# Performance work log

Measured on AMD Instinct MI355X. Metric: run time of the kernel, lower is better.

## Reference

```python
import jax, jax.numpy as jnp
import numpy as np

B, S, H, V = 16, 128, 512, 50000
N, R = 5, 2          # mem_size, read_heads
Wd = H               # memory cell width
EPS = 1e-6
XI_SIZES = [R * Wd, R, Wd, 1, Wd, Wd, R, 1, 1, 3 * R]
XI = int(np.sum(XI_SIZES))  # 2573


def oneplus(x):
    return 1.0 + jax.nn.softplus(x)


def content_weight(M, k, beta):
    # M: [B,N,Wd], k: [B,R,Wd], beta: [B,R] -> [B,R,N]
    Mn = M / (jnp.linalg.norm(M, axis=-1, keepdims=True) + EPS)
    kn = k / (jnp.linalg.norm(k, axis=-1, keepdims=True) + EPS)
    sim = jnp.einsum('brw,bnw->brn', kn, Mn)
    return jax.nn.softmax(beta[:, :, None] * sim, axis=-1)


def setup_inputs() -> dict:
    key = jax.random.key(0)
    ks = jax.random.split(key, 8)
    emb = jax.random.normal(ks[0], (V, H), jnp.float32) * 0.02
    emb = emb.at[0].set(0.0)  # PAD row
    return {
        'source': jax.random.randint(ks[1], (B, S), 0, V),
        'source_lengths': jax.random.randint(ks[2], (B,), 1, S + 1),
        'emb': emb,
        'W_ih': jax.random.normal(ks[3], (4 * H, H + R * Wd), jnp.float32) * 0.02,
        'W_hh': jax.random.normal(ks[4], (4 * H, H), jnp.float32) * 0.02,
        'b_lstm': jnp.zeros((4 * H,), jnp.float32),
        'W_int': jax.random.normal(ks[5], (H, XI), jnp.float32) * 0.02,
        'b_int': jnp.zeros((XI,), jnp.float32),
        'W_out': jax.random.normal(ks[6], (H + R * Wd, H), jnp.float32) * 0.02,
        'b_out': jnp.zeros((H,), jnp.float32),
    }


def dnc_forward(source, emb, W_ih, W_hh, b_lstm, W_int, b_int, W_out, b_out):
    x_emb = emb[source]  # [B,S,H] embedding lookup
    splits = np.cumsum(XI_SIZES)[:-1]
    eye = jnp.eye(N, dtype=jnp.float32)

    def step(carry, x_t):
        h, c, M, u, p, L, wr, ww, r = carry
        # LSTM controller: input = [embedded token; read vectors]
        xin = jnp.concatenate([x_t, r.reshape(-1, R * Wd)], axis=-1)
        gates = xin @ W_ih.T + h @ W_hh.T + b_lstm
        i_, f_, g_, o_ = jnp.split(gates, 4, axis=-1)
        c = jax.nn.sigmoid(f_) * c + jax.nn.sigmoid(i_) * jnp.tanh(g_)
        h = jax.nn.sigmoid(o_) * jnp.tanh(c)
        # interface vector
        xi = h @ W_int + b_int
        (rk, rb, wk, wb, e, v, fg, ga, gw, pi) = jnp.split(xi, splits, axis=-1)
        rk = rk.reshape(-1, R, Wd)
        rb = oneplus(rb)                       # [B,R]
        wb = oneplus(wb)                       # [B,1]
        e = jax.nn.sigmoid(e)                  # [B,Wd]
        fg = jax.nn.sigmoid(fg)                # [B,R]
        ga = jax.nn.sigmoid(ga)                # [B,1]
        gw = jax.nn.sigmoid(gw)                # [B,1]
        pi = jax.nn.softmax(pi.reshape(-1, R, 3), axis=-1)
        # usage / retention
        psi = jnp.prod(1.0 - fg[:, :, None] * wr, axis=1)        # [B,N]
        u = (u + ww - u * ww) * psi
        # allocation weighting (sort-based, irregular access)
        phi = jnp.argsort(u, axis=-1)
        u_s = jnp.take_along_axis(u, phi, axis=-1)
        excl = jnp.concatenate([jnp.ones_like(u_s[:, :1]), jnp.cumprod(u_s, axis=-1)[:, :-1]], axis=-1)
        a_s = (1.0 - u_s) * excl
        a = jnp.take_along_axis(a_s, jnp.argsort(phi, axis=-1), axis=-1)
        # write weighting
        cw = content_weight(M, wk[:, None, :], wb)[:, 0]         # [B,N]
        ww = gw * (ga * a + (1.0 - ga) * cw)
        # memory write
        M = M * (1.0 - ww[:, :, None] * e[:, None, :]) + ww[:, :, None] * v[:, None, :]
        # temporal link matrix + precedence
        L = (1.0 - ww[:, :, None] - ww[:, None, :]) * L + ww[:, :, None] * p[:, None, :]
        L = L * (1.0 - eye)
        p = (1.0 - ww.sum(-1, keepdims=True)) * p + ww
        # read weightings
        fw = jnp.einsum('bij,brj->bri', L, wr)
        bw = jnp.einsum('bji,brj->bri', L, wr)
        cr = content_weight(M, rk, rb)                           # [B,R,N]
        wr = pi[..., 0:1] * bw + pi[..., 1:2] * cr + pi[..., 2:3] * fw
        r = jnp.einsum('brn,bnw->brw', wr, M)                    # [B,R,Wd]
        out_t = jnp.concatenate([h, r.reshape(-1, R * Wd)], axis=-1) @ W_out + b_out
        return (h, c, M, u, p, L, wr, ww, r), out_t

    z = jnp.zeros
    init = (z((B, H)), z((B, H)), z((B, N, Wd)), z((B, N)), z((B, N)),
            z((B, N, N)), z((B, R, N)), z((B, N)), z((B, R, Wd)))
    (h, c, *_), outs = jax.lax.scan(step, init, jnp.swapaxes(x_emb, 0, 1))
    return jnp.swapaxes(outs, 0, 1), h, c


def reference(source, source_lengths, emb, W_ih, W_hh, b_lstm, W_int, b_int, W_out, b_out):
    outputs, h, c = dnc_forward(source, emb, W_ih, W_hh, b_lstm, W_int, b_int, W_out, b_out)
    return outputs, (h, c)
```

## Files before the change

kernel.cpp:

```cpp
#include <hip/hip_runtime.h>
#include <math.h>

#define EPSC 1e-6f
#define NBLK 128

#define OFF_H     0u
#define OFF_R     16384u
#define OFF_FLAGS 32768u
#define OFF_GO    36864u
#define STATE_END 40960u
#define OFF_XI    40960u
#define OFF_GX    90112u
#define OFF_HR    4284416u

typedef float f32x4 __attribute__((ext_vector_type(4)));

__device__ __forceinline__ float sigmf(float x) { return 1.0f / (1.0f + expf(-x)); }
__device__ __forceinline__ float oneplusf(float x) {
    return 1.0f + fmaxf(x, 0.0f) + log1pf(expf(-fabsf(x)));
}

__device__ __forceinline__ void gst(float* p, float v) {
    __hip_atomic_store((unsigned*)p, __float_as_uint(v),
                       __ATOMIC_RELAXED, __HIP_MEMORY_SCOPE_AGENT);
}

__device__ __forceinline__ void cld12(
    f32x4& d0, f32x4& d1, f32x4& d2, f32x4& d3, f32x4& d4, f32x4& d5,
    f32x4& d6, f32x4& d7, f32x4& d8, f32x4& d9, f32x4& d10, f32x4& d11,
    const float* p0, const float* p1, const float* p2, const float* p3,
    const float* p4, const float* p5, const float* p6, const float* p7,
    const float* p8, const float* p9, const float* p10, const float* p11)
{
    asm volatile(
        "global_load_dwordx4 %0, %12, off sc0 sc1\n\t"
        "global_load_dwordx4 %1, %13, off sc0 sc1\n\t"
        "global_load_dwordx4 %2, %14, off sc0 sc1\n\t"
        "global_load_dwordx4 %3, %15, off sc0 sc1\n\t"
        "global_load_dwordx4 %4, %16, off sc0 sc1\n\t"
        "global_load_dwordx4 %5, %17, off sc0 sc1\n\t"
        "global_load_dwordx4 %6, %18, off sc0 sc1\n\t"
        "global_load_dwordx4 %7, %19, off sc0 sc1\n\t"
        "global_load_dwordx4 %8, %20, off sc0 sc1\n\t"
        "global_load_dwordx4 %9, %21, off sc0 sc1\n\t"
        "global_load_dwordx4 %10, %22, off sc0 sc1\n\t"
        "global_load_dwordx4 %11, %23, off sc0 sc1\n\t"
        "s_waitcnt vmcnt(0)"
        : "=&v"(d0), "=&v"(d1), "=&v"(d2), "=&v"(d3), "=&v"(d4), "=&v"(d5),
          "=&v"(d6), "=&v"(d7), "=&v"(d8), "=&v"(d9), "=&v"(d10), "=&v"(d11)
        : "v"(p0), "v"(p1), "v"(p2), "v"(p3), "v"(p4), "v"(p5),
          "v"(p6), "v"(p7), "v"(p8), "v"(p9), "v"(p10), "v"(p11)
        : "memory");
}

__device__ __forceinline__ void cld8(
    f32x4& d0, f32x4& d1, f32x4& d2, f32x4& d3,
    f32x4& d4, f32x4& d5, f32x4& d6, f32x4& d7,
    const float* p0, const float* p1, const float* p2, const float* p3,
    const float* p4, const float* p5, const float* p6, const float* p7)
{
    asm volatile(
        "global_load_dwordx4 %0, %8, off sc0 sc1\n\t"
        "global_load_dwordx4 %1, %9, off sc0 sc1\n\t"
        "global_load_dwordx4 %2, %10, off sc0 sc1\n\t"
        "global_load_dwordx4 %3, %11, off sc0 sc1\n\t"
        "global_load_dwordx4 %4, %12, off sc0 sc1\n\t"
        "global_load_dwordx4 %5, %13, off sc0 sc1\n\t"
        "global_load_dwordx4 %6, %14, off sc0 sc1\n\t"
        "global_load_dwordx4 %7, %15, off sc0 sc1\n\t"
        "s_waitcnt vmcnt(0)"
        : "=&v"(d0), "=&v"(d1), "=&v"(d2), "=&v"(d3),
          "=&v"(d4), "=&v"(d5), "=&v"(d6), "=&v"(d7)
        : "v"(p0), "v"(p1), "v"(p2), "v"(p3),
          "v"(p4), "v"(p5), "v"(p6), "v"(p7)
        : "memory");
}

__device__ __forceinline__ void cld3(
    f32x4& d0, f32x4& d1, f32x4& d2,
    const float* p0, const float* p1, const float* p2)
{
    asm volatile(
        "global_load_dwordx4 %0, %3, off sc0 sc1\n\t"
        "global_load_dwordx4 %1, %4, off sc0 sc1\n\t"
        "global_load_dwordx4 %2, %5, off sc0 sc1\n\t"
        "s_waitcnt vmcnt(0)"
        : "=&v"(d0), "=&v"(d1), "=&v"(d2)
        : "v"(p0), "v"(p1), "v"(p2)
        : "memory");
}

__device__ __forceinline__ void gsync(unsigned* flags, unsigned* go, unsigned gen,
                                      int bi, int tid)
{
    __builtin_amdgcn_s_waitcnt(0);
    __syncthreads();
    if (tid == 0)
        __hip_atomic_store(&flags[bi * 32], gen, __ATOMIC_RELAXED, __HIP_MEMORY_SCOPE_AGENT);
    if (bi == 0) {
        if (tid < NBLK) {
            unsigned v;
            do {
                v = __hip_atomic_load(&flags[tid * 32], __ATOMIC_RELAXED, __HIP_MEMORY_SCOPE_AGENT);
                if (v < gen) __builtin_amdgcn_s_sleep(1);
            } while (v < gen);
        }
        __syncthreads();
        if (tid < NBLK)
            __hip_atomic_store(&go[tid * 32], gen, __ATOMIC_RELAXED, __HIP_MEMORY_SCOPE_AGENT);
    }
    if (tid == 0) {
        unsigned v;
        do {
            v = __hip_atomic_load(&go[bi * 32], __ATOMIC_RELAXED, __HIP_MEMORY_SCOPE_AGENT);
            if (v < gen) __builtin_amdgcn_s_sleep(1);
        } while (v < gen);
    }
    __syncthreads();
}

template <int K>
__device__ __forceinline__ void blk_reduce(float* v, float (*s_red)[20],
                                           float* outp, int tid)
{
#pragma unroll
    for (int i = 0; i < K; i++) {
        float x = v[i];
        for (int o = 32; o > 0; o >>= 1) x += __shfl_down(x, o, 64);
        if ((tid & 63) == 0) s_red[tid >> 6][i] = x;
    }
    __syncthreads();
    if (tid < K) outp[tid] = s_red[0][tid] + s_red[1][tid] + s_red[2][tid] + s_red[3][tid];
    __syncthreads();
}

__global__ __launch_bounds__(256, 1) void k_main(
    const float* __restrict__ W_ih, const float* __restrict__ W_hh,
    const float* __restrict__ W_int, const float* __restrict__ b_int,
    const float* __restrict__ gx, float* __restrict__ hbuf,
    float* __restrict__ rbuf, float* __restrict__ xib,
    float* __restrict__ hr, float* __restrict__ out,
    unsigned* __restrict__ flags, unsigned* __restrict__ go)
{
    const int tid = threadIdx.x;
    const int bi  = blockIdx.x;

    __shared__ __align__(16) float big_u[12288];
    __shared__ float s_part[1024];
    __shared__ float c_s[64];
    __shared__ __align__(16) float s_M[5][520];
    __shared__ float st_u[5], st_p[5], st_L[25], st_wr[10], st_ww[5];
    __shared__ float s_red[4][20];
    __shared__ float s_rb[2], s_wb, s_fg[2], s_ga, s_gw, s_pi[2][3];
    __shared__ float s_wrold[2][5], s_uu[5], s_a[5], s_wwn[5];
    __shared__ float s_pold[5], s_Lnew[25];
    __shared__ float s_zw[5], s_z[2][5], s_fw[2][5], s_bw[2][5];
    __shared__ float s_dotA[11], s_dotB[17], s_wrnew[2][5];

    const int cG  = tid & 15;
    const int ksl = tid >> 4;
    const int cg  = (cG >> 2) * 512 + bi * 4 + (cG & 3);

    if (tid < 64) c_s[tid] = 0.f;
    if (bi < 16) {
        for (int i = tid; i < 5 * 520; i += 256) (&s_M[0][0])[i] = 0.f;
        if (tid < 5)  { st_u[tid] = 0.f; st_p[tid] = 0.f; st_ww[tid] = 0.f; }
        if (tid < 25) st_L[tid] = 0.f;
        if (tid < 10) st_wr[tid] = 0.f;
    }
    __syncthreads();

    unsigned gen = 0;

#pragma unroll 1
    for (int t = 0; t < 128; t++) {
        const float* h_in  = hbuf + (t & 1) * 8192;
        float*       h_out = hbuf + ((t + 1) & 1) * 8192;

        float acc[16];
#pragma unroll
        for (int b = 0; b < 16; b++) acc[b] = 0.f;

#pragma unroll 1
        for (int hf = 0; hf < 2; hf++) {
            {
                const int b  = tid >> 4;
                const int sg = tid & 15;
                const float* pp[12];
#pragma unroll
                for (int i = 0; i < 12; i++) {
                    int kg = hf * 768 + sg * 4 + i * 64;
                    pp[i] = (kg < 512) ? h_in + b * 512 + kg
                                       : rbuf + b * 1024 + (kg - 512);
                }
                f32x4 d0, d1, d2, d3, d4, d5, d6, d7, d8, d9, d10, d11;
                cld12(d0, d1, d2, d3, d4, d5, d6, d7, d8, d9, d10, d11,
                      pp[0], pp[1], pp[2], pp[3], pp[4], pp[5],
                      pp[6], pp[7], pp[8], pp[9], pp[10], pp[11]);
                float* dst = &big_u[b * 768 + sg * 4];
                *(f32x4*)(dst + 0 * 64) = d0;  *(f32x4*)(dst + 1 * 64) = d1;
                *(f32x4*)(dst + 2 * 64) = d2;  *(f32x4*)(dst + 3 * 64) = d3;
                *(f32x4*)(dst + 4 * 64) = d4;  *(f32x4*)(dst + 5 * 64) = d5;
                *(f32x4*)(dst + 6 * 64) = d6;  *(f32x4*)(dst + 7 * 64) = d7;
                *(f32x4*)(dst + 8 * 64) = d8;  *(f32x4*)(dst + 9 * 64) = d9;
                *(f32x4*)(dst + 10 * 64) = d10; *(f32x4*)(dst + 11 * 64) = d11;
            }
            __syncthreads();
#pragma unroll
            for (int i = 0; i < 12; i++) {
                int lc = ksl * 4 + i * 64;
                int kg = hf * 768 + lc;
                const float* wp = (kg < 512) ? W_hh + (size_t)cg * 512 + kg
                                             : W_ih + (size_t)cg * 1536 + kg;
                f32x4 wv = *(const f32x4*)wp;
#pragma unroll
                for (int b = 0; b < 16; b++) {
                    f32x4 xv = *(const f32x4*)&big_u[b * 768 + lc];
                    acc[b] = fmaf(wv[0], xv[0], acc[b]);
                    acc[b] = fmaf(wv[1], xv[1], acc[b]);
                    acc[b] = fmaf(wv[2], xv[2], acc[b]);
                    acc[b] = fmaf(wv[3], xv[3], acc[b]);
                }
            }
            __syncthreads();
        }

#pragma unroll
        for (int b = 0; b < 16; b++) {
            float x = acc[b];
            x += __shfl_xor(x, 16, 64);
            x += __shfl_xor(x, 32, 64);
            acc[b] = x;
        }
        {
            int wv = tid >> 6;
            if ((tid & 63) < 16) {
#pragma unroll
                for (int b = 0; b < 16; b++)
                    s_part[(wv * 16 + cG) * 16 + b] = acc[b];
            }
        }
        __syncthreads();
        {
            int c = tid & 15, b = tid >> 4;
            float tot = s_part[(0 * 16 + c) * 16 + b] + s_part[(1 * 16 + c) * 16 + b]
                      + s_part[(2 * 16 + c) * 16 + b] + s_part[(3 * 16 + c) * 16 + b];
            int cgc = (c >> 2) * 512 + bi * 4 + (c & 3);
            tot += gx[((size_t)t * 16 + b) * 2048 + cgc];
            s_part[c * 16 + b] = tot;
        }
        __syncthreads();
        if (tid < 64) {
            int jl = tid & 3, b = tid >> 2;
            float gi  = s_part[(0 * 4 + jl) * 16 + b];
            float gf  = s_part[(1 * 4 + jl) * 16 + b];
            float gg  = s_part[(2 * 4 + jl) * 16 + b];
            float go_ = s_part[(3 * 4 + jl) * 16 + b];
            float cc = sigmf(gf) * c_s[jl * 16 + b] + sigmf(gi) * tanhf(gg);
            float hh = sigmf(go_) * tanhf(cc);
            c_s[jl * 16 + b] = cc;
            int j = bi * 4 + jl;
            gst(h_out + b * 512 + j, hh);
            hr[((size_t)t * 16 + b) * 1536 + j] = hh;
            if (t == 127) {
                out[1048576 + b * 512 + j] = hh;
                out[1048576 + 8192 + b * 512 + j] = cc;
            }
        }
        gen++;
        gsync(flags, go, gen, bi, tid);

        {
            {
                const int b = tid >> 4, s = tid & 15;
                const float* hp = h_out + b * 512 + s * 4;
                f32x4 d0, d1, d2, d3, d4, d5, d6, d7;
                cld8(d0, d1, d2, d3, d4, d5, d6, d7,
                     hp + 0 * 64, hp + 1 * 64, hp + 2 * 64, hp + 3 * 64,
                     hp + 4 * 64, hp + 5 * 64, hp + 6 * 64, hp + 7 * 64);
                float* dst = &big_u[b * 512 + s * 4];
                *(f32x4*)(dst + 0 * 64) = d0; *(f32x4*)(dst + 1 * 64) = d1;
                *(f32x4*)(dst + 2 * 64) = d2; *(f32x4*)(dst + 3 * 64) = d3;
                *(f32x4*)(dst + 4 * 64) = d4; *(f32x4*)(dst + 5 * 64) = d5;
                *(f32x4*)(dst + 6 * 64) = d6; *(f32x4*)(dst + 7 * 64) = d7;
            }
            __syncthreads();
            const int ql  = tid & 15;
            const int kcl = tid >> 4;
#pragma unroll 1
            for (int p = 0; p < 2; p++) {
                int q0 = p * 2048 + bi * 16;
                if (p == 1 && q0 >= 2573) break;
                int q  = q0 + ql;
                int qc = (q < 2573) ? q : 2572;
                float wxr[32];
#pragma unroll
                for (int i = 0; i < 32; i++)
                    wxr[i] = W_int[(size_t)(kcl * 32 + i) * 2573 + qc];
                float ax[16];
#pragma unroll
                for (int b = 0; b < 16; b++) ax[b] = 0.f;
#pragma unroll
                for (int b = 0; b < 16; b++) {
                    const f32x4* hp = (const f32x4*)&big_u[b * 512 + kcl * 32];
#pragma unroll
                    for (int i4 = 0; i4 < 8; i4++) {
                        f32x4 hv = hp[i4];
                        ax[b] = fmaf(wxr[i4 * 4 + 0], hv[0], ax[b]);
                        ax[b] = fmaf(wxr[i4 * 4 + 1], hv[1], ax[b]);
                        ax[b] = fmaf(wxr[i4 * 4 + 2], hv[2], ax[b]);
                        ax[b] = fmaf(wxr[i4 * 4 + 3], hv[3], ax[b]);
                    }
                }
#pragma unroll
                for (int b = 0; b < 16; b++) {
                    float x = ax[b];
                    x += __shfl_xor(x, 16, 64);
                    x += __shfl_xor(x, 32, 64);
                    ax[b] = x;
                }
                {
                    int wv = tid >> 6;
                    if ((tid & 63) < 16) {
#pragma unroll
                        for (int b = 0; b < 16; b++)
                            s_part[(wv * 16 + ql) * 16 + b] = ax[b];
                    }
                }
                __syncthreads();
                {
                    int q_l = tid >> 4, b = tid & 15;
                    int qq = q0 + q_l;
                    if (qq < 2573) {
                        float v = s_part[(0 + q_l) * 16 + b] + s_part[(16 + q_l) * 16 + b]
                                + s_part[(32 + q_l) * 16 + b] + s_part[(48 + q_l) * 16 + b]
                                + b_int[qq];
                        gst(&xib[b * 3072 + qq], v);
                    }
                }
                __syncthreads();
            }
        }
        gen++;
        gsync(flags, go, gen, bi, tid);

        if (bi < 16) {
            {
                const float* xs = xib + bi * 3072;
                f32x4 d0, d1, d2;
                cld3(d0, d1, d2,
                     xs + (tid + 0) * 4, xs + (tid + 256) * 4, xs + (tid + 512) * 4);
                *(f32x4*)&big_u[(tid + 0) * 4]   = d0;
                *(f32x4*)&big_u[(tid + 256) * 4] = d1;
                *(f32x4*)&big_u[(tid + 512) * 4] = d2;
            }
            __syncthreads();
            const float* xb = big_u;

            if (tid == 0) {
                s_wb = oneplusf(xb[1538]);
                s_ga = sigmf(xb[2565]);
                s_gw = sigmf(xb[2566]);
            }
            if (tid == 1 || tid == 2) {
                int rr = tid - 1;
                s_rb[rr] = oneplusf(xb[1024 + rr]);
                s_fg[rr] = sigmf(xb[2563 + rr]);
                float z0 = xb[2567 + rr * 3], z1 = xb[2568 + rr * 3], z2 = xb[2569 + rr * 3];
                float mx = fmaxf(z0, fmaxf(z1, z2));
                float e0 = expf(z0 - mx), e1 = expf(z1 - mx), e2 = expf(z2 - mx);
                float s = e0 + e1 + e2;
                s_pi[rr][0] = e0 / s; s_pi[rr][1] = e1 / s; s_pi[rr][2] = e2 / s;
            }
            if (tid >= 32 && tid < 42) { int i = tid - 32; s_wrold[i / 5][i % 5] = st_wr[i]; }
            if (tid >= 64 && tid < 69) { s_pold[tid - 64] = st_p[tid - 64]; }
            __syncthreads();
            if (tid < 5) {
                float psi = (1.f - s_fg[0] * s_wrold[0][tid]) * (1.f - s_fg[1] * s_wrold[1][tid]);
                float un = (st_u[tid] + st_ww[tid] - st_u[tid] * st_ww[tid]) * psi;
                s_uu[tid] = un; st_u[tid] = un;
            }
            __syncthreads();
            if (tid < 5) {
                float excl = 1.f;
#pragma unroll
                for (int m2 = 0; m2 < 5; m2++) {
                    bool before = (s_uu[m2] < s_uu[tid]) || (s_uu[m2] == s_uu[tid] && m2 < tid);
                    if (before) excl *= s_uu[m2];
                }
                s_a[tid] = (1.f - s_uu[tid]) * excl;
            }
            float accA[11];
#pragma unroll
            for (int i = 0; i < 11; i++) accA[i] = 0.f;
            for (int w = tid; w < 512; w += 256) {
                float wk = xb[1026 + w];
                accA[10] += wk * wk;
#pragma unroll
                for (int n = 0; n < 5; n++) {
                    float m_ = s_M[n][w];
                    accA[n]     += m_ * m_;
                    accA[5 + n] += wk * m_;
                }
            }
            blk_reduce<11>(accA, s_red, s_dotA, tid);
            if (tid < 5) {
                float sim = s_dotA[5 + tid] /
                            ((sqrtf(s_dotA[10]) + EPSC) * (sqrtf(s_dotA[tid]) + EPSC));
                s_zw[tid] = s_wb * sim;
            }
            __syncthreads();
            if (tid < 5) {
                float mx = s_zw[0];
#pragma unroll
                for (int m2 = 1; m2 < 5; m2++) mx = fmaxf(mx, s_zw[m2]);
                float sum = 0.f;
#pragma unroll
                for (int m2 = 0; m2 < 5; m2++) sum += expf(s_zw[m2] - mx);
                float cw = expf(s_zw[tid] - mx) / sum;
                float w_ = s_gw * (s_ga * s_a[tid] + (1.f - s_ga) * cw);
                s_wwn[tid] = w_; st_ww[tid] = w_;
            }
            __syncthreads();
            float accB[17];
#pragma unroll
            for (int i = 0; i < 17; i++) accB[i] = 0.f;
            for (int w = tid; w < 512; w += 256) {
                float ew = sigmf(xb[1539 + w]);
                float vw = xb[2051 + w];
                float rk0 = xb[w], rk1 = xb[512 + w];
                accB[15] += rk0 * rk0; accB[16] += rk1 * rk1;
#pragma unroll
                for (int n = 0; n < 5; n++) {
                    float m_ = s_M[n][w];
                    float mn_ = m_ * (1.f - s_wwn[n] * ew) + s_wwn[n] * vw;
                    s_M[n][w] = mn_;
                    accB[n]      += mn_ * mn_;
                    accB[5 + n]  += rk0 * mn_;
                    accB[10 + n] += rk1 * mn_;
                }
            }
            blk_reduce<17>(accB, s_red, s_dotB, tid);
            if (tid < 25) {
                int i2 = tid / 5, j2 = tid % 5;
                float Ln = (i2 == j2) ? 0.f
                         : (1.f - s_wwn[i2] - s_wwn[j2]) * st_L[tid] + s_wwn[i2] * s_pold[j2];
                s_Lnew[tid] = Ln; st_L[tid] = Ln;
            }
            __syncthreads();
            if (tid < 5) {
                float wsum = s_wwn[0] + s_wwn[1] + s_wwn[2] + s_wwn[3] + s_wwn[4];
                st_p[tid] = (1.f - wsum) * s_pold[tid] + s_wwn[tid];
            }
            if (tid < 10) {
                int rr = tid / 5, ii = tid % 5;
                float fw = 0.f, bw = 0.f;
#pragma unroll
                for (int j2 = 0; j2 < 5; j2++) {
                    fw += s_Lnew[ii * 5 + j2] * s_wrold[rr][j2];
                    bw += s_Lnew[j2 * 5 + ii] * s_wrold[rr][j2];
                }
                s_fw[rr][ii] = fw; s_bw[rr][ii] = bw;
                float sim = s_dotB[5 + rr * 5 + ii] /
                            ((sqrtf(s_dotB[15 + rr]) + EPSC) * (sqrtf(s_dotB[ii]) + EPSC));
                s_z[rr][ii] = s_rb[rr] * sim;
            }
            __syncthreads();
            if (tid < 10) {
                int rr = tid / 5, ii = tid % 5;
                float mx = s_z[rr][0];
#pragma unroll
                for (int m2 = 1; m2 < 5; m2++) mx = fmaxf(mx, s_z[rr][m2]);
                float sum = 0.f;
#pragma unroll
                for (int m2 = 0; m2 < 5; m2++) sum += expf(s_z[rr][m2] - mx);
                float cr = expf(s_z[rr][ii] - mx) / sum;
                float wn = s_pi[rr][0] * s_bw[rr][ii] + s_pi[rr][1] * cr + s_pi[rr][2] * s_fw[rr][ii];
                s_wrnew[rr][ii] = wn; st_wr[rr * 5 + ii] = wn;
            }
            __syncthreads();
            for (int idx = tid; idx < 1024; idx += 256) {
                int rr = idx >> 9, w = idx & 511;
                float rv = 0.f;
#pragma unroll
                for (int n = 0; n < 5; n++) rv += s_wrnew[rr][n] * s_M[n][w];
                gst(&rbuf[bi * 1024 + idx], rv);
                hr[((size_t)t * 16 + bi) * 1536 + 512 + idx] = rv;
            }
        }
        gen++;
        gsync(flags, go, gen, bi, tid);
    }
}

__global__ __launch_bounds__(256) void k_embgx(
    const int* __restrict__ src, const float* __restrict__ emb,
    const float* __restrict__ W_ih, const float* __restrict__ b_lstm,
    float* __restrict__ gx)
{
    __shared__ __align__(16) float As[16][68];
    __shared__ __align__(16) float Bs[16][68];
    const int tid = threadIdx.x;
    const int bm = blockIdx.x, bn = blockIdx.y;
    const int tm = tid >> 4, tn = tid & 15;
    float acc[4][4] = {};
    for (int k0 = 0; k0 < 512; k0 += 16) {
#pragma unroll
        for (int i = 0; i < 4; i++) {
            int idx = tid + 256 * i;
            int m = idx >> 4, kk = idx & 15;
            int tok = bm * 64 + m;
            int row = src[(tok & 15) * 128 + (tok >> 4)];
            As[kk][m] = emb[(size_t)row * 512 + k0 + kk];
        }
#pragma unroll
        for (int i = 0; i < 4; i++) {
            int idx = tid + 256 * i;
            int n = idx >> 4, kk = idx & 15;
            Bs[kk][n] = W_ih[(size_t)(bn * 64 + n) * 1536 + k0 + kk];
        }
        __syncthreads();
#pragma unroll
        for (int kk = 0; kk < 16; kk++) {
            float4 av = *(const float4*)&As[kk][tm * 4];
            float4 bv = *(const float4*)&Bs[kk][tn * 4];
            float a[4] = {av.x, av.y, av.z, av.w};
            float b[4] = {bv.x, bv.y, bv.z, bv.w};
#pragma unroll
            for (int i = 0; i < 4; i++)
#pragma unroll
                for (int j = 0; j < 4; j++) acc[i][j] = fmaf(a[i], b[j], acc[i][j]);
        }
        __syncthreads();
    }
#pragma unroll
    for (int i = 0; i < 4; i++) {
        int tok = bm * 64 + tm * 4 + i;
#pragma unroll
        for (int j = 0; j < 4; j++) {
            int col = bn * 64 + tn * 4 + j;
            gx[(size_t)tok * 2048 + col] = acc[i][j] + b_lstm[col];
        }
    }
}

__global__ __launch_bounds__(256) void k_out(
    const float* __restrict__ hr, const float* __restrict__ W_out,
    const float* __restrict__ b_out, float* __restrict__ out)
{
    __shared__ __align__(16) float As[16][68];
    __shared__ __align__(16) float Bs[16][68];
    const int tid = threadIdx.x;
    const int bm = blockIdx.x, bn = blockIdx.y;
    const int tm = tid >> 4, tn = tid & 15;
    float acc[4][4] = {};
    for (int k0 = 0; k0 < 1536; k0 += 16) {
#pragma unroll
        for (int i = 0; i < 4; i++) {
            int idx = tid + 256 * i;
            int m = idx >> 4, kk = idx & 15;
            As[kk][m] = hr[(size_t)(bm * 64 + m) * 1536 + k0 + kk];
        }
#pragma unroll
        for (int i = 0; i < 4; i++) {
            int idx = tid + 256 * i;
            int kk = idx >> 6, n = idx & 63;
            Bs[kk][n] = W_out[(size_t)(k0 + kk) * 512 + bn * 64 + n];
        }
        __syncthreads();
#pragma unroll
        for (int kk = 0; kk < 16; kk++) {
            float4 av = *(const float4*)&As[kk][tm * 4];
            float4 bv = *(const float4*)&Bs[kk][tn * 4];
            float a[4] = {av.x, av.y, av.z, av.w};
            float b[4] = {bv.x, bv.y, bv.z, bv.w};
#pragma unroll
            for (int i = 0; i < 4; i++)
#pragma unroll
                for (int j = 0; j < 4; j++) acc[i][j] = fmaf(a[i], b[j], acc[i][j]);
        }
        __syncthreads();
    }
#pragma unroll
    for (int i = 0; i < 4; i++) {
        int tok = bm * 64 + tm * 4 + i;
        int b_ = tok & 15, s_ = tok >> 4;
#pragma unroll
        for (int j = 0; j < 4; j++) {
            int qn = bn * 64 + tn * 4 + j;
            out[(size_t)((b_ << 7) + s_) * 512 + qn] = acc[i][j] + b_out[qn];
        }
    }
}

extern "C" void kernel_launch(void* const* d_in, const int* in_sizes, int n_in,
                              void* d_out, int out_size, void* d_ws, size_t ws_size,
                              hipStream_t stream)
{
    const int*   src    = (const int*)d_in[0];
    const float* emb    = (const float*)d_in[2];
    const float* W_ih   = (const float*)d_in[3];
    const float* W_hh   = (const float*)d_in[4];
    const float* b_lstm = (const float*)d_in[5];
    const float* W_int  = (const float*)d_in[6];
    const float* b_int  = (const float*)d_in[7];
    const float* W_out  = (const float*)d_in[8];
    const float* b_out  = (const float*)d_in[9];

    float* ws  = (float*)d_ws;
    float* out = (float*)d_out;

    float*    hbuf  = ws + OFF_H;
    float*    rbuf  = ws + OFF_R;
    unsigned* flags = (unsigned*)(ws + OFF_FLAGS);
    unsigned* go    = (unsigned*)(ws + OFF_GO);
    float*    xib   = ws + OFF_XI;
    float*    gx    = ws + OFF_GX;
    float*    hrb   = ws + OFF_HR;

    hipMemsetAsync(ws, 0, STATE_END * sizeof(float), stream);

    k_embgx<<<dim3(32, 32), 256, 0, stream>>>(src, emb, W_ih, b_lstm, gx);

    k_main<<<dim3(NBLK), dim3(256), 0, stream>>>(
        W_ih, W_hh, W_int, b_int, gx, hbuf, rbuf, xib, hrb, out, flags, go);

    k_out<<<dim3(32, 8), 256, 0, stream>>>(hrb, W_out, b_out, out);
}
```

Baseline: 4.440 ms.

## Replace grid barrier with per-block flags and single-pass padded LSTM gate staging

The grid-wide barrier after the interface projection is replaced by per-block progress flags. Only the 16 memory-update blocks spin on those flags, and the other blocks continue without waiting. The LSTM gate matvec now stages the whole h and r input into padded shared memory in one pass instead of two halves, which drops two block syncs per step and uses bank-conflict-avoiding strides. The gx value is prefetched early, and the leftover interface columns are reassigned to the tail blocks for balance. Shared memory use grows and the hand-rolled flag protocol adds ordering risk.

```diff
diff --git a/kernel.cpp b/kernel.cpp
--- a/kernel.cpp
+++ b/kernel.cpp
@@ -8,10 +8,11 @@
 #define OFF_R     16384u
 #define OFF_FLAGS 32768u
 #define OFF_GO    36864u
-#define STATE_END 40960u
-#define OFF_XI    40960u
-#define OFF_GX    90112u
-#define OFF_HR    4284416u
+#define OFF_XF    40960u
+#define STATE_END 45056u
+#define OFF_XI    45056u
+#define OFF_GX    94208u
+#define OFF_HR    4288512u
 
 typedef float f32x4 __attribute__((ext_vector_type(4)));
 
@@ -25,54 +26,74 @@
                        __ATOMIC_RELAXED, __HIP_MEMORY_SCOPE_AGENT);
 }
 
-__device__ __forceinline__ void cld12(
-    f32x4& d0, f32x4& d1, f32x4& d2, f32x4& d3, f32x4& d4, f32x4& d5,
-    f32x4& d6, f32x4& d7, f32x4& d8, f32x4& d9, f32x4& d10, f32x4& d11,
-    const float* p0, const float* p1, const float* p2, const float* p3,
-    const float* p4, const float* p5, const float* p6, const float* p7,
-    const float* p8, const float* p9, const float* p10, const float* p11)
+__device__ __forceinline__ void ld8_nw(
+    f32x4& d0, f32x4& d1, f32x4& d2, f32x4& d3,
+    f32x4& d4, f32x4& d5, f32x4& d6, f32x4& d7, const float* p)
 {
     asm volatile(
-        "global_load_dwordx4 %0, %12, off sc0 sc1\n\t"
-        "global_load_dwordx4 %1, %13, off sc0 sc1\n\t"
-        "global_load_dwordx4 %2, %14, off sc0 sc1\n\t"
-        "global_load_dwordx4 %3, %15, off sc0 sc1\n\t"
-        "global_load_dwordx4 %4, %16, off sc0 sc1\n\t"
-        "global_load_dwordx4 %5, %17, off sc0 sc1\n\t"
-        "global_load_dwordx4 %6, %18, off sc0 sc1\n\t"
-        "global_load_dwordx4 %7, %19, off sc0 sc1\n\t"
-        "global_load_dwordx4 %8, %20, off sc0 sc1\n\t"
-        "global_load_dwordx4 %9, %21, off sc0 sc1\n\t"
-        "global_load_dwordx4 %10, %22, off sc0 sc1\n\t"
-        "global_load_dwordx4 %11, %23, off sc0 sc1\n\t"
-        "s_waitcnt vmcnt(0)"
-        : "=&v"(d0), "=&v"(d1), "=&v"(d2), "=&v"(d3), "=&v"(d4), "=&v"(d5),
-          "=&v"(d6), "=&v"(d7), "=&v"(d8), "=&v"(d9), "=&v"(d10), "=&v"(d11)
-        : "v"(p0), "v"(p1), "v"(p2), "v"(p3), "v"(p4), "v"(p5),
-          "v"(p6), "v"(p7), "v"(p8), "v"(p9), "v"(p10), "v"(p11)
+        "global_load_dwordx4 %0, %8, off sc0 sc1\n\t"
+        "global_load_dwordx4 %1, %8, off offset:256 sc0 sc1\n\t"
+        "global_load_dwordx4 %2, %8, off offset:512 sc0 sc1\n\t"
+        "global_load_dwordx4 %3, %8, off offset:768 sc0 sc1\n\t"
+        "global_load_dwordx4 %4, %8, off offset:1024 sc0 sc1\n\t"
+        "global_load_dwordx4 %5, %8, off offset:1280 sc0 sc1\n\t"
+        "global_load_dwordx4 %6, %8, off offset:1536 sc0 sc1\n\t"
+        "global_load_dwordx4 %7, %8, off offset:1792 sc0 sc1"
+        : "=&v"(d0), "=&v"(d1), "=&v"(d2), "=&v"(d3),
+          "=&v"(d4), "=&v"(d5), "=&v"(d6), "=&v"(d7)
+        : "v"(p)
         : "memory");
 }
 
-__device__ __forceinline__ void cld8(
+__device__ __forceinline__ void ld16_w(
     f32x4& d0, f32x4& d1, f32x4& d2, f32x4& d3,
     f32x4& d4, f32x4& d5, f32x4& d6, f32x4& d7,
-    const float* p0, const float* p1, const float* p2, const float* p3,
-    const float* p4, const float* p5, const float* p6, const float* p7)
+    f32x4& d8, f32x4& d9, f32x4& d10, f32x4& d11,
+    f32x4& d12, f32x4& d13, f32x4& d14, f32x4& d15, const float* p)
+{
+    asm volatile(
+        "global_load_dwordx4 %0, %16, off sc0 sc1\n\t"
+        "global_load_dwordx4 %1, %16, off offset:256 sc0 sc1\n\t"
+        "global_load_dwordx4 %2, %16, off offset:512 sc0 sc1\n\t"
+        "global_load_dwordx4 %3, %16, off offset:768 sc0 sc1\n\t"
+        "global_load_dwordx4 %4, %16, off offset:1024 sc0 sc1\n\t"
+        "global_load_dwordx4 %5, %16, off offset:1280 sc0 sc1\n\t"
+        "global_load_dwordx4 %6, %16, off offset:1536 sc0 sc1\n\t"
+        "global_load_dwordx4 %7, %16, off offset:1792 sc0 sc1\n\t"
+        "global_load_dwordx4 %8, %16, off offset:2048 sc0 sc1\n\t"
+        "global_load_dwordx4 %9, %16, off offset:2304 sc0 sc1\n\t"
+        "global_load_dwordx4 %10, %16, off offset:2560 sc0 sc1\n\t"
+        "global_load_dwordx4 %11, %16, off offset:2816 sc0 sc1\n\t"
+        "global_load_dwordx4 %12, %16, off offset:3072 sc0 sc1\n\t"
+        "global_load_dwordx4 %13, %16, off offset:3328 sc0 sc1\n\t"
+        "global_load_dwordx4 %14, %16, off offset:3584 sc0 sc1\n\t"
+        "global_load_dwordx4 %15, %16, off offset:3840 sc0 sc1\n\t"
+        "s_waitcnt vmcnt(0)"
+        : "=&v"(d0), "=&v"(d1), "=&v"(d2), "=&v"(d3),
+          "=&v"(d4), "=&v"(d5), "=&v"(d6), "=&v"(d7),
+          "=&v"(d8), "=&v"(d9), "=&v"(d10), "=&v"(d11),
+          "=&v"(d12), "=&v"(d13), "=&v"(d14), "=&v"(d15)
+        : "v"(p)
+        : "memory");
+}
+
+__device__ __forceinline__ void ld8_w(
+    f32x4& d0, f32x4& d1, f32x4& d2, f32x4& d3,
+    f32x4& d4, f32x4& d5, f32x4& d6, f32x4& d7, const float* p)
 {
     asm volatile(
         "global_load_dwordx4 %0, %8, off sc0 sc1\n\t"
-        "global_load_dwordx4 %1, %9, off sc0 sc1\n\t"
-        "global_load_dwordx4 %2, %10, off sc0 sc1\n\t"
-        "global_load_dwordx4 %3, %11, off sc0 sc1\n\t"
-        "global_load_dwordx4 %4, %12, off sc0 sc1\n\t"
-        "global_load_dwordx4 %5, %13, off sc0 sc1\n\t"
-        "global_load_dwordx4 %6, %14, off sc0 sc1\n\t"
-        "global_load_dwordx4 %7, %15, off sc0 sc1\n\t"
+        "global_load_dwordx4 %1, %8, off offset:256 sc0 sc1\n\t"
+        "global_load_dwordx4 %2, %8, off offset:512 sc0 sc1\n\t"
+        "global_load_dwordx4 %3, %8, off offset:768 sc0 sc1\n\t"
+        "global_load_dwordx4 %4, %8, off offset:1024 sc0 sc1\n\t"
+        "global_load_dwordx4 %5, %8, off offset:1280 sc0 sc1\n\t"
+        "global_load_dwordx4 %6, %8, off offset:1536 sc0 sc1\n\t"
+        "global_load_dwordx4 %7, %8, off offset:1792 sc0 sc1\n\t"
         "s_waitcnt vmcnt(0)"
         : "=&v"(d0), "=&v"(d1), "=&v"(d2), "=&v"(d3),
           "=&v"(d4), "=&v"(d5), "=&v"(d6), "=&v"(d7)
-        : "v"(p0), "v"(p1), "v"(p2), "v"(p3),
-          "v"(p4), "v"(p5), "v"(p6), "v"(p7)
+        : "v"(p)
         : "memory");
 }
 
@@ -140,13 +161,15 @@
     const float* __restrict__ gx, float* __restrict__ hbuf,
     float* __restrict__ rbuf, float* __restrict__ xib,
     float* __restrict__ hr, float* __restrict__ out,
-    unsigned* __restrict__ flags, unsigned* __restrict__ go)
+    unsigned* __restrict__ flags, unsigned* __restrict__ go,
+    unsigned* __restrict__ xf)
 {
     const int tid = threadIdx.x;
     const int bi  = blockIdx.x;
 
-    __shared__ __align__(16) float big_u[12288];
+    __shared__ __align__(16) float big_u[27008];
     __shared__ float s_part[1024];
+    __shared__ float s_tot[256];
     __shared__ float c_s[64];
     __shared__ __align__(16) float s_M[5][520];
     __shared__ float st_u[5], st_p[5], st_L[25], st_wr[10], st_ww[5];
@@ -157,10 +180,6 @@
     __shared__ float s_zw[5], s_z[2][5], s_fw[2][5], s_bw[2][5];
     __shared__ float s_dotA[11], s_dotB[17], s_wrnew[2][5];
 
-    const int cG  = tid & 15;
-    const int ksl = tid >> 4;
-    const int cg  = (cG >> 2) * 512 + bi * 4 + (cG & 3);
-
     if (tid < 64) c_s[tid] = 0.f;
     if (bi < 16) {
         for (int i = tid; i < 5 * 520; i += 256) (&s_M[0][0])[i] = 0.f;
@@ -177,54 +196,62 @@
         const float* h_in  = hbuf + (t & 1) * 8192;
         float*       h_out = hbuf + ((t + 1) & 1) * 8192;
 
+        float gxv;
+        {
+            int c = tid & 15, b = tid >> 4;
+            int cgc = (c >> 2) * 512 + bi * 4 + (c & 3);
+            gxv = gx[((size_t)t * 16 + b) * 2048 + cgc];
+        }
+
+        {
+            const int b = tid >> 4, sg = tid & 15;
+            const float* ph = h_in + b * 512 + sg * 4;
+            const float* pr = rbuf + b * 1024 + sg * 4;
+            f32x4 h0, h1, h2, h3, h4, h5, h6, h7;
+            f32x4 r0, r1, r2, r3, r4, r5, r6, r7, r8, r9, r10, r11, r12, r13, r14, r15;
+            ld8_nw(h0, h1, h2, h3, h4, h5, h6, h7, ph);
+            ld16_w(r0, r1, r2, r3, r4, r5, r6, r7,
+                   r8, r9, r10, r11, r12, r13, r14, r15, pr);
+#define STG(kk, D) { int k = (kk); int cc = k / 48; \
+                     *(f32x4*)&big_u[b * 1688 + cc * 52 + (k - cc * 48)] = D; }
+            STG(sg * 4 + 0 * 64, h0)  STG(sg * 4 + 1 * 64, h1)
+            STG(sg * 4 + 2 * 64, h2)  STG(sg * 4 + 3 * 64, h3)
+            STG(sg * 4 + 4 * 64, h4)  STG(sg * 4 + 5 * 64, h5)
+            STG(sg * 4 + 6 * 64, h6)  STG(sg * 4 + 7 * 64, h7)
+            STG(512 + sg * 4 + 0 * 64, r0)   STG(512 + sg * 4 + 1 * 64, r1)
+            STG(512 + sg * 4 + 2 * 64, r2)   STG(512 + sg * 4 + 3 * 64, r3)
+            STG(512 + sg * 4 + 4 * 64, r4)   STG(512 + sg * 4 + 5 * 64, r5)
+            STG(512 + sg * 4 + 6 * 64, r6)   STG(512 + sg * 4 + 7 * 64, r7)
+            STG(512 + sg * 4 + 8 * 64, r8)   STG(512 + sg * 4 + 9 * 64, r9)
+            STG(512 + sg * 4 + 10 * 64, r10) STG(512 + sg * 4 + 11 * 64, r11)
+            STG(512 + sg * 4 + 12 * 64, r12) STG(512 + sg * 4 + 13 * 64, r13)
+            STG(512 + sg * 4 + 14 * 64, r14) STG(512 + sg * 4 + 15 * 64, r15)
+#undef STG
+        }
+        __syncthreads();
+
+        const int cG  = tid & 15;
+        const int ksG = tid >> 4;
+        const int cg  = (cG >> 2) * 512 + bi * 4 + (cG & 3);
         float acc[16];
 #pragma unroll
         for (int b = 0; b < 16; b++) acc[b] = 0.f;
-
-#pragma unroll 1
-        for (int hf = 0; hf < 2; hf++) {
-            {
-                const int b  = tid >> 4;
-                const int sg = tid & 15;
-                const float* pp[12];
-#pragma unroll
-                for (int i = 0; i < 12; i++) {
-                    int kg = hf * 768 + sg * 4 + i * 64;
-                    pp[i] = (kg < 512) ? h_in + b * 512 + kg
-                                       : rbuf + b * 1024 + (kg - 512);
-                }
-                f32x4 d0, d1, d2, d3, d4, d5, d6, d7, d8, d9, d10, d11;
-                cld12(d0, d1, d2, d3, d4, d5, d6, d7, d8, d9, d10, d11,
-                      pp[0], pp[1], pp[2], pp[3], pp[4], pp[5],
-                      pp[6], pp[7], pp[8], pp[9], pp[10], pp[11]);
-                float* dst = &big_u[b * 768 + sg * 4];
-                *(f32x4*)(dst + 0 * 64) = d0;  *(f32x4*)(dst + 1 * 64) = d1;
-                *(f32x4*)(dst + 2 * 64) = d2;  *(f32x4*)(dst + 3 * 64) = d3;
-                *(f32x4*)(dst + 4 * 64) = d4;  *(f32x4*)(dst + 5 * 64) = d5;
-                *(f32x4*)(dst + 6 * 64) = d6;  *(f32x4*)(dst + 7 * 64) = d7;
-                *(f32x4*)(dst + 8 * 64) = d8;  *(f32x4*)(dst + 9 * 64) = d9;
-                *(f32x4*)(dst + 10 * 64) = d10; *(f32x4*)(dst + 11 * 64) = d11;
-            }
-            __syncthreads();
-#pragma unroll
-            for (int i = 0; i < 12; i++) {
-                int lc = ksl * 4 + i * 64;
-                int kg = hf * 768 + lc;
-                const float* wp = (kg < 512) ? W_hh + (size_t)cg * 512 + kg
-                                             : W_ih + (size_t)cg * 1536 + kg;
-                f32x4 wv = *(const f32x4*)wp;
-#pragma unroll
-                for (int b = 0; b < 16; b++) {
-                    f32x4 xv = *(const f32x4*)&big_u[b * 768 + lc];
-                    acc[b] = fmaf(wv[0], xv[0], acc[b]);
-                    acc[b] = fmaf(wv[1], xv[1], acc[b]);
-                    acc[b] = fmaf(wv[2], xv[2], acc[b]);
-                    acc[b] = fmaf(wv[3], xv[3], acc[b]);
-                }
-            }
-            __syncthreads();
-        }
-
+#pragma unroll
+        for (int i = 0; i < 24; i++) {
+            int kg = ksG * 96 + i * 4;
+            const float* wp = (kg < 512) ? W_hh + (size_t)cg * 512 + kg
+                                         : W_ih + (size_t)cg * 1536 + kg;
+            f32x4 wv = *(const f32x4*)wp;
+            int lo = ksG * 104 + ((i < 12) ? i * 4 : 52 + (i - 12) * 4);
+#pragma unroll
+            for (int b = 0; b < 16; b++) {
+                f32x4 xv = *(const f32x4*)&big_u[b * 1688 + lo];
+                acc[b] = fmaf(wv[0], xv[0], acc[b]);
+                acc[b] = fmaf(wv[1], xv[1], acc[b]);
+                acc[b] = fmaf(wv[2], xv[2], acc[b]);
+                acc[b] = fmaf(wv[3], xv[3], acc[b]);
+            }
+        }
 #pragma unroll
         for (int b = 0; b < 16; b++) {
             float x = acc[b];
@@ -243,19 +270,18 @@
         __syncthreads();
         {
             int c = tid & 15, b = tid >> 4;
-            float tot = s_part[(0 * 16 + c) * 16 + b] + s_part[(1 * 16 + c) * 16 + b]
-                      + s_part[(2 * 16 + c) * 16 + b] + s_part[(3 * 16 + c) * 16 + b];
-            int cgc = (c >> 2) * 512 + bi * 4 + (c & 3);
-            tot += gx[((size_t)t * 16 + b) * 2048 + cgc];
-            s_part[c * 16 + b] = tot;
+            float tot = gxv;
+#pragma unroll
+            for (int w = 0; w < 4; w++) tot += s_part[(w * 16 + c) * 16 + b];
+            s_tot[c * 16 + b] = tot;
         }
         __syncthreads();
         if (tid < 64) {
             int jl = tid & 3, b = tid >> 2;
-            float gi  = s_part[(0 * 4 + jl) * 16 + b];
-            float gf  = s_part[(1 * 4 + jl) * 16 + b];
-            float gg  = s_part[(2 * 4 + jl) * 16 + b];
-            float go_ = s_part[(3 * 4 + jl) * 16 + b];
+            float gi  = s_tot[(0 * 4 + jl) * 16 + b];
+            float gf  = s_tot[(1 * 4 + jl) * 16 + b];
+            float gg  = s_tot[(2 * 4 + jl) * 16 + b];
+            float go_ = s_tot[(3 * 4 + jl) * 16 + b];
             float cc = sigmf(gf) * c_s[jl * 16 + b] + sigmf(gi) * tanhf(gg);
             float hh = sigmf(go_) * tanhf(cc);
             c_s[jl * 16 + b] = cc;
@@ -273,24 +299,22 @@
         {
             {
                 const int b = tid >> 4, s = tid & 15;
-                const float* hp = h_out + b * 512 + s * 4;
-                f32x4 d0, d1, d2, d3, d4, d5, d6, d7;
-                cld8(d0, d1, d2, d3, d4, d5, d6, d7,
-                     hp + 0 * 64, hp + 1 * 64, hp + 2 * 64, hp + 3 * 64,
-                     hp + 4 * 64, hp + 5 * 64, hp + 6 * 64, hp + 7 * 64);
-                float* dst = &big_u[b * 512 + s * 4];
-                *(f32x4*)(dst + 0 * 64) = d0; *(f32x4*)(dst + 1 * 64) = d1;
-                *(f32x4*)(dst + 2 * 64) = d2; *(f32x4*)(dst + 3 * 64) = d3;
-                *(f32x4*)(dst + 4 * 64) = d4; *(f32x4*)(dst + 5 * 64) = d5;
-                *(f32x4*)(dst + 6 * 64) = d6; *(f32x4*)(dst + 7 * 64) = d7;
+                const float* ph = h_out + b * 512 + s * 4;
+                f32x4 e0, e1, e2, e3, e4, e5, e6, e7;
+                ld8_w(e0, e1, e2, e3, e4, e5, e6, e7, ph);
+#define STX(j, E) { int k = s * 4 + (j) * 64; \
+                    *(f32x4*)&big_u[b * 592 + (k >> 5) * 36 + (k & 31)] = E; }
+                STX(0, e0) STX(1, e1) STX(2, e2) STX(3, e3)
+                STX(4, e4) STX(5, e5) STX(6, e6) STX(7, e7)
+#undef STX
             }
             __syncthreads();
             const int ql  = tid & 15;
             const int kcl = tid >> 4;
 #pragma unroll 1
             for (int p = 0; p < 2; p++) {
-                int q0 = p * 2048 + bi * 16;
-                if (p == 1 && q0 >= 2573) break;
+                if (p == 1 && bi < 95) break;
+                int q0 = (p == 0) ? bi * 16 : 2048 + (bi - 95) * 16;
                 int q  = q0 + ql;
                 int qc = (q < 2573) ? q : 2572;
                 float wxr[32];
@@ -302,7 +326,7 @@
                 for (int b = 0; b < 16; b++) ax[b] = 0.f;
 #pragma unroll
                 for (int b = 0; b < 16; b++) {
-                    const f32x4* hp = (const f32x4*)&big_u[b * 512 + kcl * 32];
+                    const f32x4* hp = (const f32x4*)&big_u[b * 592 + kcl * 36];
 #pragma unroll
                     for (int i4 = 0; i4 < 8; i4++) {
                         f32x4 hv = hp[i4];
@@ -332,19 +356,32 @@
                     int q_l = tid >> 4, b = tid & 15;
                     int qq = q0 + q_l;
                     if (qq < 2573) {
-                        float v = s_part[(0 + q_l) * 16 + b] + s_part[(16 + q_l) * 16 + b]
-                                + s_part[(32 + q_l) * 16 + b] + s_part[(48 + q_l) * 16 + b]
-                                + b_int[qq];
+                        float v = b_int[qq];
+#pragma unroll
+                        for (int w = 0; w < 4; w++)
+                            v += s_part[(w * 16 + q_l) * 16 + b];
                         gst(&xib[b * 3072 + qq], v);
                     }
                 }
                 __syncthreads();
             }
         }
-        gen++;
-        gsync(flags, go, gen, bi, tid);
+        __builtin_amdgcn_s_waitcnt(0);
+        __syncthreads();
+        if (tid == 0)
+            __hip_atomic_store(&xf[bi * 32], (unsigned)(t + 1),
+                               __ATOMIC_RELAXED, __HIP_MEMORY_SCOPE_AGENT);
 
         if (bi < 16) {
+            if (tid < 128) {
+                unsigned v;
+                do {
+                    v = __hip_atomic_load(&xf[tid * 32], __ATOMIC_RELAXED,
+                                          __HIP_MEMORY_SCOPE_AGENT);
+                    if (v < (unsigned)(t + 1)) __builtin_amdgcn_s_sleep(2);
+                } while (v < (unsigned)(t + 1));
+            }
+            __syncthreads();
             {
                 const float* xs = xib + bi * 3072;
                 f32x4 d0, d1, d2;
@@ -614,6 +651,7 @@
     float*    rbuf  = ws + OFF_R;
     unsigned* flags = (unsigned*)(ws + OFF_FLAGS);
     unsigned* go    = (unsigned*)(ws + OFF_GO);
+    unsigned* xf    = (unsigned*)(ws + OFF_XF);
     float*    xib   = ws + OFF_XI;
     float*    gx    = ws + OFF_GX;
     float*    hrb   = ws + OFF_HR;
@@ -623,7 +661,7 @@
     k_embgx<<<dim3(32, 32), 256, 0, stream>>>(src, emb, W_ih, b_lstm, gx);
 
     k_main<<<dim3(NBLK), dim3(256), 0, stream>>>(
-        W_ih, W_hh, W_int, b_int, gx, hbuf, rbuf, xib, hrb, out, flags, go);
+        W_ih, W_hh, W_int, b_int, gx, hbuf, rbuf, xib, hrb, out, flags, go, xf);
 
     k_out<<<dim3(32, 8), 256, 0, stream>>>(hrb, W_out, b_out, out);
 }
```

New measurement: 4.622 ms. 1.04x slower.
